# Optimization experiments

Measured on AMD Instinct MI355X. Metric: run time of the kernel, lower is better.

Reference implementation:

```python
import jax, jax.numpy as jnp
import numpy as np

D_MODEL = 768
N_HEADS = 4
HEAD_DIM = D_MODEL // N_HEADS


def setup_inputs() -> dict:
    key = jax.random.key(0)
    ks = jax.random.split(key, 9)
    B, S = 4, 2048
    scale = 1.0 / np.sqrt(D_MODEL)
    inputs = jax.random.normal(ks[0], (B, S, D_MODEL), dtype=jnp.float32)
    # Linear weights stored as [in, out] for x @ W + b
    Wq = jax.random.normal(ks[1], (D_MODEL, D_MODEL), dtype=jnp.float32) * scale
    bq = jnp.zeros((D_MODEL,), dtype=jnp.float32)
    Wk = jax.random.normal(ks[2], (D_MODEL, D_MODEL), dtype=jnp.float32) * scale
    bk = jnp.zeros((D_MODEL,), dtype=jnp.float32)
    Wv = jax.random.normal(ks[3], (D_MODEL, D_MODEL), dtype=jnp.float32) * scale
    bv = jnp.zeros((D_MODEL,), dtype=jnp.float32)
    Wo = jax.random.normal(ks[4], (D_MODEL, D_MODEL), dtype=jnp.float32) * scale
    bo = jnp.zeros((D_MODEL,), dtype=jnp.float32)
    return {"inputs": inputs, "Wq": Wq, "bq": bq, "Wk": Wk, "bk": bk,
            "Wv": Wv, "bv": bv, "Wo": Wo, "bo": bo}


def reference(inputs, Wq, bq, Wk, bk, Wv, bv, Wo, bo):
    B, S, _ = inputs.shape
    H, Dh = N_HEADS, HEAD_DIM
    # projections -> [B, H, S, Dh]
    def split_heads(x):
        return x.reshape(B, S, H, Dh).transpose(0, 2, 1, 3)
    Q = split_heads(inputs @ Wq + bq)
    K = split_heads(inputs @ Wk + bk)
    V = split_heads(inputs @ Wv + bv)
    scores = jnp.einsum('bhqd,bhkd->bhqk', Q, K) / jnp.sqrt(jnp.float32(Dh))
    causal = jnp.tril(jnp.ones((S, S), dtype=bool))  # True = keep
    scores = jnp.where(causal, scores, -jnp.inf)
    weights = jax.nn.softmax(scores, axis=-1)
    # dropout is identity in eval mode
    ctx = jnp.einsum('bhqk,bhkd->bhqd', weights, V)
    ctx = ctx.transpose(0, 2, 1, 3).reshape(B, S, H * Dh)
    return ctx @ Wo + bo
```

## Files before the change

kernel.cpp:

```cpp
#include <hip/hip_runtime.h>
#include <hip/hip_bf16.h>
#include <cstddef>

typedef __attribute__((ext_vector_type(8))) short short8;
typedef __attribute__((ext_vector_type(4))) float f32x4;
typedef __attribute__((ext_vector_type(4))) unsigned short u16x4;

#define D_MODEL 768
#define N_HEADS 4
#define HEAD_DIM 192
#define BATCH 4
#define SEQ 2048
#define M_ROWS (BATCH*SEQ)

__device__ __forceinline__ short f2bf(float f) {
  union { float f; unsigned u; } v; v.f = f;
  unsigned r = v.u + 0x7FFFu + ((v.u >> 16) & 1u);
  return (short)(r >> 16);
}

__device__ __forceinline__ float fexp2(float x) {
  return __builtin_amdgcn_exp2f(x);
}

__device__ __forceinline__ void gl_lds16(const void* g, void* l) {
  __builtin_amdgcn_global_load_lds(
      (const __attribute__((address_space(1))) void*)g,
      (__attribute__((address_space(3))) void*)l, 16, 0, 0);
}

__global__ __launch_bounds__(256) void cast_kernel(const float* __restrict__ src,
                                                   short* __restrict__ dst, int n8) {
  int i = blockIdx.x * 256 + threadIdx.x;
  if (i >= n8) return;
  const float4* s = (const float4*)src;
  float4 a = s[2 * i], b = s[2 * i + 1];
  short8 o;
  o[0] = f2bf(a.x); o[1] = f2bf(a.y); o[2] = f2bf(a.z); o[3] = f2bf(a.w);
  o[4] = f2bf(b.x); o[5] = f2bf(b.y); o[6] = f2bf(b.z); o[7] = f2bf(b.w);
  *(short8*)(dst + (size_t)i * 8) = o;
}

__global__ __launch_bounds__(256) void wtrans(const float* __restrict__ W,
                                              short* __restrict__ Wt) {
  __shared__ float tile[32][33];
  int k0 = blockIdx.x * 32, n0 = blockIdx.y * 32;
  int tc = threadIdx.x & 31, tr = threadIdx.x >> 5;
#pragma unroll
  for (int i = 0; i < 4; i++)
    tile[tr + i * 8][tc] = W[(size_t)(k0 + tr + i * 8) * D_MODEL + n0 + tc];
  __syncthreads();
#pragma unroll
  for (int i = 0; i < 4; i++)
    Wt[(size_t)(n0 + tr + i * 8) * D_MODEL + k0 + tc] = f2bf(tile[tc][tr + i * 8]);
}

__global__ __launch_bounds__(256) void bias_concat(const float* __restrict__ a,
                                                   const float* __restrict__ b,
                                                   const float* __restrict__ c,
                                                   float* __restrict__ dst) {
  int i = blockIdx.x * 256 + threadIdx.x;
  if (i >= 3 * D_MODEL) return;
  float v = i < 768 ? a[i] : (i < 1536 ? b[i - 768] : c[i - 1536]);
  dst[i] = v;
}

template <int MODE>
__global__ __launch_bounds__(256, 4) void gemm_bf16(const short* __restrict__ A,
                                                    const short* __restrict__ Wt,
                                                    const float* __restrict__ bias,
                                                    short* __restrict__ oQ,
                                                    short* __restrict__ oK,
                                                    short* __restrict__ oV,
                                                    float* __restrict__ oF, int N) {
  __shared__ short As[128 * 64];
  __shared__ short Bs[128 * 64];
  const int K = 768;
  const int m0 = blockIdx.x * 128, n0 = blockIdx.y * 128;
  const int t = threadIdx.x, lane = t & 63, w = t >> 6;
  const int wr = w >> 1, wc = w & 1, lr = lane & 15, lg = lane >> 4;

  f32x4 acc[4][4] = {};

  for (int k0 = 0; k0 < K; k0 += 64) {
#pragma unroll
    for (int i = 0; i < 4; i++) {
      int id = w * 4 + i;
      int row = id * 8 + (lane >> 3);
      int cc = (lane & 7) ^ (row & 7);
      gl_lds16(A + (size_t)(m0 + row) * K + k0 + cc * 8, As + id * 512);
      gl_lds16(Wt + (size_t)(n0 + row) * K + k0 + cc * 8, Bs + id * 512);
    }
    __syncthreads();
#pragma unroll
    for (int kb = 0; kb < 2; kb++) {
      short8 a[4], b[4];
#pragma unroll
      for (int m = 0; m < 4; m++) {
        int row = wr * 64 + m * 16 + lr;
        a[m] = *(const short8*)&As[row * 64 + (((kb * 4 + lg) ^ (row & 7)) << 3)];
      }
#pragma unroll
      for (int n = 0; n < 4; n++) {
        int row = wc * 64 + n * 16 + lr;
        b[n] = *(const short8*)&Bs[row * 64 + (((kb * 4 + lg) ^ (row & 7)) << 3)];
      }
#pragma unroll
      for (int m = 0; m < 4; m++)
#pragma unroll
        for (int n = 0; n < 4; n++)
          acc[m][n] = __builtin_amdgcn_mfma_f32_16x16x32_bf16(a[m], b[n], acc[m][n], 0, 0, 0);
    }
    __syncthreads();
  }

  if (MODE == 0) {
#pragma unroll
    for (int m = 0; m < 4; m++)
#pragma unroll
      for (int n = 0; n < 4; n++) {
        int col = n0 + wc * 64 + n * 16 + lr;
        float bv = bias[col];
#pragma unroll
        for (int r = 0; r < 4; r++) {
          int row = m0 + wr * 64 + m * 16 + lg * 4 + r;
          oF[(size_t)row * N + col] = acc[m][n][r] + bv;
        }
      }
  } else {
    const int bb = m0 >> 11;
#pragma unroll
    for (int m = 0; m < 4; m++) {
      int s0 = (m0 & (SEQ - 1)) + wr * 64 + m * 16 + lg * 4;
#pragma unroll
      for (int n = 0; n < 4; n++) {
        int col = n0 + wc * 64 + n * 16 + lr;
        int seg = col / 768;
        int d = col - seg * 768;
        int h = d / HEAD_DIM, dd = d - h * HEAD_DIM;
        int bh = bb * N_HEADS + h;
        float bv = bias[col];
        if (seg < 2) {
          short* dst = seg == 0 ? oQ : oK;
#pragma unroll
          for (int r = 0; r < 4; r++)
            dst[((size_t)bh * SEQ + s0 + r) * HEAD_DIM + dd] = f2bf(acc[m][n][r] + bv);
        } else {
          u16x4 pk;
#pragma unroll
          for (int r = 0; r < 4; r++) pk[r] = (unsigned short)f2bf(acc[m][n][r] + bv);
          *(u16x4*)&oV[((size_t)bh * HEAD_DIM + dd) * SEQ + s0] = pk;
        }
      }
    }
  }
}

__device__ __forceinline__ void stage_kv(const short* Kp, const short* Vp, int kbase,
                                         short* KsB, short* VsB, int w, int lane) {
#pragma unroll
  for (int i = 0; i < 6; i++) {
    int id = w * 6 + i;
    int o16 = id * 64 + lane;
    int row = o16 / 24, cc0 = o16 - row * 24;
    int cc = cc0 ^ (row & 7);
    gl_lds16(Kp + (size_t)(kbase + row) * HEAD_DIM + cc * 8, KsB + id * 512);
  }
#pragma unroll
  for (int i = 0; i < 6; i++) {
    int id = w * 6 + i;
    int o16 = id * 64 + lane;
    int row = o16 >> 3, cc = (o16 & 7) ^ (row & 7);
    gl_lds16(Vp + (size_t)row * SEQ + kbase + cc * 8, VsB + id * 512);
  }
}

__global__ __launch_bounds__(256, 1) void attn_kernel(const short* __restrict__ Q,
                                                      const short* __restrict__ Kg,
                                                      const short* __restrict__ Vt,
                                                      short* __restrict__ ctx) {
  __shared__ short Ks[2][64 * 192];
  __shared__ short Vs[2][192 * 64];
  __shared__ short Ps[4][16 * 72];

  const int n = blockIdx.x;
  const int slot = n >> 3;
  const int bh = (n & 7) * 2 + (slot >> 4);
  const int p = slot & 15;
  const int b = bh >> 2, h = bh & 3;
  const short* Qp = Q + (size_t)bh * SEQ * HEAD_DIM;
  const short* Kp = Kg + (size_t)bh * SEQ * HEAD_DIM;
  const short* Vp = Vt + (size_t)bh * HEAD_DIM * SEQ;
  const int t = threadIdx.x, lane = t & 63, w = t >> 6;
  const int lr = lane & 15, lg = lane >> 4;
  const float scale2 = 0.07216878364870322f * 1.4426950408889634f;

  for (int pass = 0; pass < 2; pass++) {
    const int qt = (pass == 0) ? p : 31 - p;
    const int nkb = qt + 1;
    const int qrow_w = qt * 64 + w * 16;

    short8 qf[6];
#pragma unroll
    for (int c = 0; c < 6; c++)
      qf[c] = *(const short8*)&Qp[(size_t)(qrow_w + lr) * HEAD_DIM + c * 32 + lg * 8];

    f32x4 o[12] = {};
    float m2[4], l[4], alpha[4];
#pragma unroll
    for (int j = 0; j < 4; j++) { m2[j] = -3.0e38f; l[j] = 0.f; }

    stage_kv(Kp, Vp, 0, Ks[0], Vs[0], w, lane);

    for (int kb = 0; kb < nkb; kb++) {
      const int cur = kb & 1;
      const int kbase = kb * 64;
      if (kb + 1 < nkb) {
        stage_kv(Kp, Vp, kbase + 64, Ks[cur ^ 1], Vs[cur ^ 1], w, lane);
        asm volatile("s_waitcnt vmcnt(12)" ::: "memory");
      } else {
        asm volatile("s_waitcnt vmcnt(0)" ::: "memory");
      }
      __builtin_amdgcn_s_barrier();
      asm volatile("" ::: "memory");

      const short* Kc = Ks[cur];
      const short* Vc = Vs[cur];

      f32x4 sc[4] = {};
#pragma unroll
      for (int kc = 0; kc < 4; kc++) {
        int row = kc * 16 + lr;
        int rsw = row & 7;
#pragma unroll
        for (int c = 0; c < 6; c++) {
          short8 bfr = *(const short8*)&Kc[row * 192 + (((c * 4 + lg) ^ rsw) << 3)];
          sc[kc] = __builtin_amdgcn_mfma_f32_16x16x32_bf16(qf[c], bfr, sc[kc], 0, 0, 0);
        }
      }

#pragma unroll
      for (int j = 0; j < 4; j++) {
        int qrow = qrow_w + lg * 4 + j;
        float v[4];
#pragma unroll
        for (int kc = 0; kc < 4; kc++) {
          int col = kbase + kc * 16 + lr;
          v[kc] = (col <= qrow) ? sc[kc][j] * scale2 : -3.0e38f;
        }
        float mx = fmaxf(fmaxf(v[0], v[1]), fmaxf(v[2], v[3]));
#pragma unroll
        for (int s2 = 1; s2 < 16; s2 <<= 1) mx = fmaxf(mx, __shfl_xor(mx, s2, 64));
        float mn = fmaxf(m2[j], mx);
        alpha[j] = fexp2(m2[j] - mn);
        m2[j] = mn;
        float rs = 0.f;
#pragma unroll
        for (int kc = 0; kc < 4; kc++) {
          float e = fexp2(v[kc] - mn);
          rs += e;
          Ps[w][(lg * 4 + j) * 72 + kc * 16 + lr] = f2bf(e);
        }
#pragma unroll
        for (int s2 = 1; s2 < 16; s2 <<= 1) rs += __shfl_xor(rs, s2, 64);
        l[j] = l[j] * alpha[j] + rs;
      }
#pragma unroll
      for (int dd = 0; dd < 12; dd++)
#pragma unroll
        for (int j = 0; j < 4; j++) o[dd][j] *= alpha[j];

#pragma unroll
      for (int kb32 = 0; kb32 < 2; kb32++) {
        short8 pa = *(const short8*)&Ps[w][lr * 72 + kb32 * 32 + lg * 8];
#pragma unroll
        for (int dd = 0; dd < 12; dd++) {
          int row = dd * 16 + lr;
          short8 vb = *(const short8*)&Vc[row * 64 + (((kb32 * 4 + lg) ^ (row & 7)) << 3)];
          o[dd] = __builtin_amdgcn_mfma_f32_16x16x32_bf16(pa, vb, o[dd], 0, 0, 0);
        }
      }
      asm volatile("" ::: "memory");
      __builtin_amdgcn_s_barrier();
    }

#pragma unroll
    for (int j = 0; j < 4; j++) {
      int qrow = qrow_w + lg * 4 + j;
      float rl = 1.0f / l[j];
#pragma unroll
      for (int dd = 0; dd < 12; dd++) {
        int col = h * HEAD_DIM + dd * 16 + lr;
        ctx[((size_t)b * SEQ + qrow) * D_MODEL + col] = f2bf(o[dd][j] * rl);
      }
    }
    __builtin_amdgcn_s_barrier();
  }
}

extern "C" void kernel_launch(void* const* d_in, const int* in_sizes, int n_in,
                              void* d_out, int out_size, void* d_ws, size_t ws_size,
                              hipStream_t stream) {
  const float* X  = (const float*)d_in[0];
  const float* Wq = (const float*)d_in[1];
  const float* bq = (const float*)d_in[2];
  const float* Wk = (const float*)d_in[3];
  const float* bk = (const float*)d_in[4];
  const float* Wv = (const float*)d_in[5];
  const float* bv = (const float*)d_in[6];
  const float* Wo = (const float*)d_in[7];
  const float* bo = (const float*)d_in[8];

  char* ws = (char*)d_ws;
  const size_t XB = (size_t)M_ROWS * D_MODEL * 2;
  const size_t WQKV = (size_t)3 * D_MODEL * D_MODEL * 2;
  const size_t WB = (size_t)D_MODEL * D_MODEL * 2;

  short* Xb    = (short*)(ws);
  short* Wqkvt = (short*)(ws + XB);
  short* Wot   = (short*)(ws + XB + WQKV);
  float* bqkv  = (float*)(ws + XB + WQKV + WB);
  short* Qb    = (short*)(ws + XB + WQKV + WB + 12288);
  short* Kb    = (short*)(ws + XB + WQKV + WB + 12288 + XB);
  short* Vtb   = (short*)(ws + XB + WQKV + WB + 12288 + 2 * XB);
  short* Cb    = (short*)(ws + XB + WQKV + WB + 12288 + 3 * XB);

  const int n8x = M_ROWS * D_MODEL / 8;
  cast_kernel<<<(n8x + 255) / 256, 256, 0, stream>>>(X, Xb, n8x);
  dim3 tg(24, 24);
  wtrans<<<tg, 256, 0, stream>>>(Wq, Wqkvt);
  wtrans<<<tg, 256, 0, stream>>>(Wk, Wqkvt + (size_t)768 * 768);
  wtrans<<<tg, 256, 0, stream>>>(Wv, Wqkvt + (size_t)2 * 768 * 768);
  wtrans<<<tg, 256, 0, stream>>>(Wo, Wot);
  bias_concat<<<9, 256, 0, stream>>>(bq, bk, bv, bqkv);

  gemm_bf16<1><<<dim3(M_ROWS / 128, 2304 / 128), 256, 0, stream>>>(
      Xb, Wqkvt, bqkv, Qb, Kb, Vtb, nullptr, 2304);

  attn_kernel<<<256, 256, 0, stream>>>(Qb, Kb, Vtb, Cb);

  gemm_bf16<0><<<dim3(M_ROWS / 128, 768 / 128), 256, 0, stream>>>(
      Cb, Wot, bo, nullptr, nullptr, nullptr, (float*)d_out, 768);
}
```

Baseline: 162.0 us.

## Restructure attention into 32x32 MFMA with key-split warps and lazy rescale

Reworks the attention kernel so each pair of waves splits the 64-key block in halves over a 32-row query tile, using 32x32x16 MFMAs with transposed S^T=K·Q so P stays in registers (packed via cvt_pk_bf16 and lane exchange) instead of round-tripping through LDS. Adds a lazy online-softmax rescale that only rescales when the max grows by more than a threshold, skips fully masked key halves, and merges the two partial (m,l,O) states through LDS at the end. This reduces LDS traffic, per-row shuffle reductions and exp work, at the cost of an end-of-tile merge and higher register pressure.

```diff
diff --git a/kernel.cpp b/kernel.cpp
--- a/kernel.cpp
+++ b/kernel.cpp
@@ -4,6 +4,7 @@
 
 typedef __attribute__((ext_vector_type(8))) short short8;
 typedef __attribute__((ext_vector_type(4))) float f32x4;
+typedef __attribute__((ext_vector_type(16))) float f32x16;
 typedef __attribute__((ext_vector_type(4))) unsigned short u16x4;
 
 #define D_MODEL 768
@@ -181,36 +182,39 @@
                                                       short* __restrict__ ctx) {
   __shared__ short Ks[2][64 * 192];
   __shared__ short Vs[2][192 * 64];
-  __shared__ short Ps[4][16 * 72];
+  float* obuf = (float*)&Vs[0][0];
+  float* mlbuf = (float*)&Ks[0][0];
 
   const int n = blockIdx.x;
   const int slot = n >> 3;
   const int bh = (n & 7) * 2 + (slot >> 4);
   const int p = slot & 15;
-  const int b = bh >> 2, h = bh & 3;
+  const int b = bh >> 2, head = bh & 3;
   const short* Qp = Q + (size_t)bh * SEQ * HEAD_DIM;
   const short* Kp = Kg + (size_t)bh * SEQ * HEAD_DIM;
   const short* Vp = Vt + (size_t)bh * HEAD_DIM * SEQ;
   const int t = threadIdx.x, lane = t & 63, w = t >> 6;
-  const int lr = lane & 15, lg = lane >> 4;
+  const int wq = w >> 1, wk = w & 1;
+  const int l31 = lane & 31, hl = lane >> 5;
   const float scale2 = 0.07216878364870322f * 1.4426950408889634f;
 
   for (int pass = 0; pass < 2; pass++) {
-    const int qt = (pass == 0) ? p : 31 - p;
+    const int qt = pass ? 31 - p : p;
     const int nkb = qt + 1;
-    const int qrow_w = qt * 64 + w * 16;
-
-    short8 qf[6];
-#pragma unroll
-    for (int c = 0; c < 6; c++)
-      qf[c] = *(const short8*)&Qp[(size_t)(qrow_w + lr) * HEAD_DIM + c * 32 + lg * 8];
-
-    f32x4 o[12] = {};
-    float m2[4], l[4], alpha[4];
-#pragma unroll
-    for (int j = 0; j < 4; j++) { m2[j] = -3.0e38f; l[j] = 0.f; }
+    const int q0w = qt * 64 + wq * 32;
+    const int qlane = q0w + l31;
 
     stage_kv(Kp, Vp, 0, Ks[0], Vs[0], w, lane);
+
+    short8 qf[12];
+#pragma unroll
+    for (int c = 0; c < 12; c++)
+      qf[c] = *(const short8*)&Qp[(size_t)qlane * HEAD_DIM + c * 16 + hl * 8];
+
+    f32x16 oacc[6];
+#pragma unroll
+    for (int d = 0; d < 6; d++) oacc[d] = 0.f;
+    float m = -3.0e38f, lsum = 0.f;
 
     for (int kb = 0; kb < nkb; kb++) {
       const int cur = kb & 1;
@@ -224,77 +228,131 @@
       __builtin_amdgcn_s_barrier();
       asm volatile("" ::: "memory");
 
-      const short* Kc = Ks[cur];
-      const short* Vc = Vs[cur];
-
-      f32x4 sc[4] = {};
-#pragma unroll
-      for (int kc = 0; kc < 4; kc++) {
-        int row = kc * 16 + lr;
-        int rsw = row & 7;
-#pragma unroll
-        for (int c = 0; c < 6; c++) {
-          short8 bfr = *(const short8*)&Kc[row * 192 + (((c * 4 + lg) ^ rsw) << 3)];
-          sc[kc] = __builtin_amdgcn_mfma_f32_16x16x32_bf16(qf[c], bfr, sc[kc], 0, 0, 0);
-        }
-      }
-
-#pragma unroll
-      for (int j = 0; j < 4; j++) {
-        int qrow = qrow_w + lg * 4 + j;
-        float v[4];
-#pragma unroll
-        for (int kc = 0; kc < 4; kc++) {
-          int col = kbase + kc * 16 + lr;
-          v[kc] = (col <= qrow) ? sc[kc][j] * scale2 : -3.0e38f;
-        }
-        float mx = fmaxf(fmaxf(v[0], v[1]), fmaxf(v[2], v[3]));
-#pragma unroll
-        for (int s2 = 1; s2 < 16; s2 <<= 1) mx = fmaxf(mx, __shfl_xor(mx, s2, 64));
-        float mn = fmaxf(m2[j], mx);
-        alpha[j] = fexp2(m2[j] - mn);
-        m2[j] = mn;
+      if (kbase + wk * 32 <= q0w + 31) {
+        const short* KcB = Ks[cur];
+        const short* VcB = Vs[cur];
+
+        f32x16 sacc = 0.f;
+        const int krow = wk * 32 + l31;
+        const int krb = krow * 192;
+        const int kswz = (krow & 7) << 3;
+#pragma unroll
+        for (int c = 0; c < 12; c++) {
+          short8 kf = *(const short8*)&KcB[krb + ((c * 16 + hl * 8) ^ kswz)];
+          sacc = __builtin_amdgcn_mfma_f32_32x32x16_bf16(kf, qf[c], sacc, 0, 0, 0);
+        }
+
+        float s[16];
+        const bool need_mask = (kbase + wk * 32 + 31) > q0w;
+        const int kb0 = kbase + wk * 32 + 4 * hl;
+#pragma unroll
+        for (int r = 0; r < 16; r++) {
+          float v = sacc[r] * scale2;
+          if (need_mask) {
+            int kg = kb0 + (r & 3) + 8 * (r >> 2);
+            if (kg > qlane) v = -3.0e38f;
+          }
+          s[r] = v;
+        }
+        float mx = s[0];
+#pragma unroll
+        for (int r = 1; r < 16; r++) mx = fmaxf(mx, s[r]);
+        mx = fmaxf(mx, __shfl_xor(mx, 32, 64));
+        if (!__all(mx <= m + 8.0f)) {
+          float mn = fmaxf(m, mx);
+          float al = fexp2(m - mn);
+          m = mn;
+          lsum *= al;
+#pragma unroll
+          for (int d = 0; d < 6; d++) oacc[d] *= al;
+        }
+        float pr[16];
         float rs = 0.f;
 #pragma unroll
-        for (int kc = 0; kc < 4; kc++) {
-          float e = fexp2(v[kc] - mn);
-          rs += e;
-          Ps[w][(lg * 4 + j) * 72 + kc * 16 + lr] = f2bf(e);
-        }
-#pragma unroll
-        for (int s2 = 1; s2 < 16; s2 <<= 1) rs += __shfl_xor(rs, s2, 64);
-        l[j] = l[j] * alpha[j] + rs;
-      }
-#pragma unroll
-      for (int dd = 0; dd < 12; dd++)
-#pragma unroll
-        for (int j = 0; j < 4; j++) o[dd][j] *= alpha[j];
-
-#pragma unroll
-      for (int kb32 = 0; kb32 < 2; kb32++) {
-        short8 pa = *(const short8*)&Ps[w][lr * 72 + kb32 * 32 + lg * 8];
-#pragma unroll
-        for (int dd = 0; dd < 12; dd++) {
-          int row = dd * 16 + lr;
-          short8 vb = *(const short8*)&Vc[row * 64 + (((kb32 * 4 + lg) ^ (row & 7)) << 3)];
-          o[dd] = __builtin_amdgcn_mfma_f32_16x16x32_bf16(pa, vb, o[dd], 0, 0, 0);
+        for (int r = 0; r < 16; r++) {
+          pr[r] = fexp2(s[r] - m);
+          rs += pr[r];
+        }
+        rs += __shfl_xor(rs, 32, 64);
+        lsum += rs;
+
+        unsigned pk[8], ex[8];
+#pragma unroll
+        for (int j = 0; j < 8; j++) {
+          unsigned r0;
+          asm("v_cvt_pk_bf16_f32 %0, %1, %2" : "=v"(r0) : "v"(pr[2 * j]), "v"(pr[2 * j + 1]));
+          pk[j] = r0;
+        }
+#pragma unroll
+        for (int j = 0; j < 8; j++) ex[j] = __shfl_xor((int)pk[j], 32, 64);
+        union { unsigned u[4]; short8 s8; } f0, f1;
+        f0.u[0] = hl ? ex[2] : pk[0];
+        f0.u[1] = hl ? ex[3] : pk[1];
+        f0.u[2] = hl ? pk[2] : ex[0];
+        f0.u[3] = hl ? pk[3] : ex[1];
+        f1.u[0] = hl ? ex[6] : pk[4];
+        f1.u[1] = hl ? ex[7] : pk[5];
+        f1.u[2] = hl ? pk[6] : ex[4];
+        f1.u[3] = hl ? pk[7] : ex[5];
+
+#pragma unroll
+        for (int db = 0; db < 6; db++) {
+          const int vrow = db * 32 + l31;
+          const int vrb = vrow * 64;
+          const int vswz = (vrow & 7) << 3;
+          short8 va = *(const short8*)&VcB[vrb + ((wk * 32 + hl * 8) ^ vswz)];
+          oacc[db] = __builtin_amdgcn_mfma_f32_32x32x16_bf16(va, f0.s8, oacc[db], 0, 0, 0);
+          short8 vb = *(const short8*)&VcB[vrb + ((wk * 32 + 16 + hl * 8) ^ vswz)];
+          oacc[db] = __builtin_amdgcn_mfma_f32_32x32x16_bf16(vb, f1.s8, oacc[db], 0, 0, 0);
         }
       }
       asm volatile("" ::: "memory");
       __builtin_amdgcn_s_barrier();
     }
 
-#pragma unroll
-    for (int j = 0; j < 4; j++) {
-      int qrow = qrow_w + lg * 4 + j;
-      float rl = 1.0f / l[j];
-#pragma unroll
-      for (int dd = 0; dd < 12; dd++) {
-        int col = h * HEAD_DIM + dd * 16 + lr;
-        ctx[((size_t)b * SEQ + qrow) * D_MODEL + col] = f2bf(o[dd][j] * rl);
-      }
-    }
-    __builtin_amdgcn_s_barrier();
+    __syncthreads();
+    if (wk == 1) {
+      if (lane < 32) {
+        mlbuf[wq * 64 + lane] = m;
+        mlbuf[wq * 64 + 32 + lane] = lsum;
+      }
+#pragma unroll
+      for (int db = 0; db < 6; db++)
+#pragma unroll
+        for (int g = 0; g < 4; g++) {
+          int d = db * 32 + 8 * g + 4 * hl;
+          f32x4 vv;
+          vv[0] = oacc[db][4 * g];
+          vv[1] = oacc[db][4 * g + 1];
+          vv[2] = oacc[db][4 * g + 2];
+          vv[3] = oacc[db][4 * g + 3];
+          *(f32x4*)&obuf[(wq * 32 + l31) * 192 + (d ^ ((l31 & 7) << 2))] = vv;
+        }
+    }
+    __syncthreads();
+    if (wk == 0) {
+      float m1 = mlbuf[wq * 64 + l31];
+      float l1 = mlbuf[wq * 64 + 32 + l31];
+      float ms = fmaxf(m, m1);
+      float a0 = fexp2(m - ms), a1 = fexp2(m1 - ms);
+      float lt = lsum * a0 + l1 * a1;
+      float rl = 1.0f / lt;
+#pragma unroll
+      for (int db = 0; db < 6; db++)
+#pragma unroll
+        for (int g = 0; g < 4; g++) {
+          int d = db * 32 + 8 * g + 4 * hl;
+          f32x4 rd = *(const f32x4*)&obuf[(wq * 32 + l31) * 192 + (d ^ ((l31 & 7) << 2))];
+          u16x4 pkk;
+#pragma unroll
+          for (int r2 = 0; r2 < 4; r2++) {
+            float v = (oacc[db][4 * g + r2] * a0 + rd[r2] * a1) * rl;
+            pkk[r2] = (unsigned short)f2bf(v);
+          }
+          *(u16x4*)&ctx[((size_t)b * SEQ + qlane) * D_MODEL + head * HEAD_DIM + d] = pkk;
+        }
+    }
+    __syncthreads();
   }
 }
 
```

New measurement: 154.4 us. 4.7% less time.
